# Optimization experiments

Hardware: AMD Instinct MI355X
Metric: run time of the kernel (lower is better)

Reference implementation:

```python
import jax, jax.numpy as jnp
import numpy as np

N = 50000
E = 800000
IN_DIM = 256
HID = 32
HEADS = 4
OUT_DIM = 40
NEG_SLOPE = 0.2


def gat_layer(x, src, dst, W, a_src, a_dst, b, n_nodes, heads, ch, concat):
    # x: [N, F_in], W: [F_in, heads*ch], a_src/a_dst: [heads, ch], b: [out]
    h = (x @ W).reshape(n_nodes, heads, ch)                 # [N,H,C]
    alpha_s = jnp.einsum('nhc,hc->nh', h, a_src)            # [N,H]
    alpha_d = jnp.einsum('nhc,hc->nh', h, a_dst)            # [N,H]
    e = jax.nn.leaky_relu(alpha_s[src] + alpha_d[dst], NEG_SLOPE)  # [E,H]
    # segment softmax over destination neighborhoods (self-loops guarantee nonempty)
    m = jax.ops.segment_max(e, dst, num_segments=n_nodes)   # [N,H]
    e = jnp.exp(e - m[dst])
    denom = jax.ops.segment_sum(e, dst, num_segments=n_nodes)
    alpha = e / (denom[dst] + 1e-16)                         # [E,H]
    msg = h[src] * alpha[:, :, None]                         # [E,H,C]
    out = jax.ops.segment_sum(msg, dst, num_segments=n_nodes)  # [N,H,C]
    out = out.reshape(n_nodes, heads * ch) if concat else out.mean(axis=1)
    return out + b


def setup_inputs() -> dict:
    key = jax.random.key(0)
    ks = jax.random.split(key, 10)
    x = jax.random.normal(ks[0], (N, IN_DIM), dtype=jnp.float32)
    edge_index = jax.random.randint(ks[1], (2, E), 0, N, dtype=jnp.int32)
    s1 = 1.0 / np.sqrt(IN_DIM)
    s2 = 1.0 / np.sqrt(HID * HEADS)
    return {
        'x': x,
        'edge_index': edge_index,
        'W1': jax.random.normal(ks[2], (IN_DIM, HEADS * HID), dtype=jnp.float32) * s1,
        'a_src1': jax.random.normal(ks[3], (HEADS, HID), dtype=jnp.float32) * s1,
        'a_dst1': jax.random.normal(ks[4], (HEADS, HID), dtype=jnp.float32) * s1,
        'b1': jnp.zeros((HEADS * HID,), dtype=jnp.float32),
        'W2': jax.random.normal(ks[5], (HEADS * HID, OUT_DIM), dtype=jnp.float32) * s2,
        'a_src2': jax.random.normal(ks[6], (1, OUT_DIM), dtype=jnp.float32) * s2,
        'a_dst2': jax.random.normal(ks[7], (1, OUT_DIM), dtype=jnp.float32) * s2,
        'b2': jnp.zeros((OUT_DIM,), dtype=jnp.float32),
    }


def reference(x, edge_index, W1, a_src1, a_dst1, b1, W2, a_src2, a_dst2, b2):
    # PyG GATConv adds self-loops by default
    loops = jnp.arange(N, dtype=edge_index.dtype)
    src = jnp.concatenate([edge_index[0], loops])
    dst = jnp.concatenate([edge_index[1], loops])
    h = gat_layer(x, src, dst, W1, a_src1, a_dst1, b1, N, HEADS, HID, True)
    h = jax.nn.relu(h)
    out = gat_layer(h, src, dst, W2, a_src2, a_dst2, b2, N, 1, OUT_DIM, False)
    return jax.nn.log_softmax(out, axis=1)
```

## Files before the change

### kernel.cpp

```cpp
#include <hip/hip_runtime.h>
#include <math.h>

#define N_NODES 50000
#define N_EDGES 800000
#define IN_DIM  256
#define F1      128
#define HEADS   4
#define OUT_DIM 40
#define NEG     0.2f

#define NB   391
#define CAP  3072
#define EB   4096

#define DCAP 96

typedef __attribute__((ext_vector_type(8))) short short8;
typedef __attribute__((ext_vector_type(4))) float float4v;

__device__ __forceinline__ unsigned short f2bf(float f) {
  unsigned int u = __float_as_uint(f);
  u += 0x7FFF + ((u >> 16) & 1);
  return (unsigned short)(u >> 16);
}
__device__ __forceinline__ float bf2f(unsigned short h) {
  return __uint_as_float((unsigned int)h << 16);
}
__device__ __forceinline__ float bflo(unsigned int u) { return __uint_as_float(u << 16); }
__device__ __forceinline__ float bfhi(unsigned int u) { return __uint_as_float(u & 0xffff0000u); }

__device__ __forceinline__ float lrelu(float e) { return e > 0.f ? e : e * NEG; }

__device__ __forceinline__ void gload_lds16(const void* g, void* l) {
  __builtin_amdgcn_global_load_lds(
      (const __attribute__((address_space(1))) unsigned int*)g,
      (__attribute__((address_space(3))) unsigned int*)l, 16, 0, 0);
}

__global__ __launch_bounds__(256) void bin_kernel(const int* __restrict__ ei,
                                                  int* __restrict__ gcnt,
                                                  int2* __restrict__ gbucket) {
  __shared__ int ls[EB];
  __shared__ int ld[EB];
  __shared__ int lcnt[NB];
  __shared__ int lcur[NB];
  __shared__ int gbaseS[NB];
  int tid = threadIdx.x;
  size_t base = (size_t)blockIdx.x * EB;
  for (int t = tid; t < NB; t += 256) { lcnt[t] = 0; lcur[t] = 0; }
  __syncthreads();
#pragma unroll
  for (int l = 0; l < EB / 256; l++) {
    int li = l * 256 + tid;
    size_t idx = base + li;
    int s = 0, d = -1;
    if (idx < N_EDGES) {
      s = ei[idx];
      d = ei[N_EDGES + idx];
      atomicAdd(&lcnt[d >> 7], 1);
    }
    ls[li] = s;
    ld[li] = d;
  }
  __syncthreads();
  for (int t = tid; t < NB; t += 256) gbaseS[t] = atomicAdd(&gcnt[t], lcnt[t]);
  __syncthreads();
#pragma unroll
  for (int l = 0; l < EB / 256; l++) {
    int li = l * 256 + tid;
    int d = ld[li];
    if (d >= 0) {
      int b = d >> 7;
      int r = gbaseS[b] + atomicAdd(&lcur[b], 1);
      if (r >= CAP) r = CAP - 1;
      gbucket[(size_t)b * CAP + r] = make_int2(ls[li], d);
    }
  }
}

__global__ __launch_bounds__(512) void bucketscan_kernel(const int* __restrict__ gcnt,
                                                         int* __restrict__ bbase,
                                                         int* __restrict__ row_ptr) {
  __shared__ int lds[512];
  int tid = threadIdx.x;
  int v = (tid < NB) ? gcnt[tid] : 0;
  lds[tid] = v;
  __syncthreads();
  for (int off = 1; off < 512; off <<= 1) {
    int t = (tid >= off) ? lds[tid - off] : 0;
    __syncthreads();
    lds[tid] += t;
    __syncthreads();
  }
  if (tid < NB) bbase[tid] = lds[tid] - v;
  if (tid == 0) row_ptr[N_NODES] = N_EDGES;
}

__global__ __launch_bounds__(256) void csr_kernel(const int2* __restrict__ gbucket,
                                                  const int* __restrict__ gcnt,
                                                  const int* __restrict__ bbase,
                                                  int* __restrict__ row_ptr,
                                                  int* __restrict__ col) {
  __shared__ int2 ent[CAP];
  __shared__ int hcnt[128];
  __shared__ int sc[128];
  __shared__ int cur[128];
  int b = blockIdx.x;
  int tid = threadIdx.x;
  int cnt = gcnt[b]; if (cnt > CAP) cnt = CAP;
  int base = bbase[b];
  if (tid < 128) hcnt[tid] = 0;
  __syncthreads();
  for (int i = tid; i < cnt; i += 256) {
    int2 e = gbucket[(size_t)b * CAP + i];
    ent[i] = e;
    atomicAdd(&hcnt[e.y & 127], 1);
  }
  __syncthreads();
  if (tid < 128) sc[tid] = hcnt[tid];
  __syncthreads();
  for (int off = 1; off < 128; off <<= 1) {
    int t = 0;
    if (tid < 128 && tid >= off) t = sc[tid - off];
    __syncthreads();
    if (tid < 128) sc[tid] += t;
    __syncthreads();
  }
  if (tid < 128) {
    int excl = sc[tid] - hcnt[tid];
    cur[tid] = excl;
    int node = (b << 7) + tid;
    if (node < N_NODES) row_ptr[node] = base + excl;
  }
  __syncthreads();
  for (int i = tid; i < cnt; i += 256) {
    int2 e = ent[i];
    int r = atomicAdd(&cur[e.y & 127], 1);
    col[base + r] = e.x;
  }
}

__global__ __launch_bounds__(256) void w1pack_kernel(const float* __restrict__ W1,
                                                     unsigned short* __restrict__ wHi,
                                                     unsigned short* __restrict__ wLo) {
  int tid = blockIdx.x * 256 + threadIdx.x;
  int kk = tid >> 9;
  int rest = tid & 511;
  int t = rest >> 6;
  int lane = rest & 63;
  int q = lane >> 4;
  int ln = lane & 15;
  int n = t * 16 + ln;
  unsigned int hi[4], lo[4];
#pragma unroll
  for (int jj = 0; jj < 4; jj++) {
    unsigned short h0, h1, l0, l1;
    {
      float v = W1[(kk * 32 + q * 8 + jj * 2) * F1 + n];
      h0 = f2bf(v); l0 = f2bf(v - bf2f(h0));
    }
    {
      float v = W1[(kk * 32 + q * 8 + jj * 2 + 1) * F1 + n];
      h1 = f2bf(v); l1 = f2bf(v - bf2f(h1));
    }
    hi[jj] = (unsigned int)h0 | ((unsigned int)h1 << 16);
    lo[jj] = (unsigned int)l0 | ((unsigned int)l1 << 16);
  }
  size_t base = (size_t)tid * 8;
  *(uint4*)&wHi[base] = make_uint4(hi[0], hi[1], hi[2], hi[3]);
  *(uint4*)&wLo[base] = make_uint4(lo[0], lo[1], lo[2], lo[3]);
}

__global__ __launch_bounds__(256) void gemm1_mfma_kernel(
    const float* __restrict__ x, const unsigned short* __restrict__ wHi,
    const unsigned short* __restrict__ wLo,
    const float* __restrict__ a_src, const float* __restrict__ a_dst,
    unsigned short* __restrict__ h1b, float* __restrict__ as1, float* __restrict__ ad1) {
  __shared__ short8 Bsh[2][1024];
  int tid = threadIdx.x;
  int w = tid >> 6;
  int lane = tid & 63;
  int q = lane >> 4;
  int ln = lane & 15;
  int rowBase = blockIdx.x * 64 + w * 16;
  int rowA = rowBase + ln;
  int rowAc = rowA < N_NODES ? rowA : N_NODES - 1;
  float4v acc[8];
#pragma unroll
  for (int t = 0; t < 8; t++) acc[t] = (float4v){0.f, 0.f, 0.f, 0.f};
  const short8* bhp = (const short8*)wHi;
  const short8* blp = (const short8*)wLo;

  auto prefetch = [&](int kk, int buf) {
#pragma unroll
    for (int c = 0; c < 2; c++) {
      int chunk = w * 2 + c;
      gload_lds16(bhp + (size_t)kk * 512 + chunk * 64 + lane, &Bsh[buf][chunk * 64]);
      gload_lds16(blp + (size_t)kk * 512 + chunk * 64 + lane, &Bsh[buf][512 + chunk * 64]);
    }
  };

  const float4* xbase = (const float4*)(x + (size_t)rowAc * IN_DIM + q * 8);
  float4 a0 = xbase[0];
  float4 a1 = xbase[1];
  prefetch(0, 0);
  __syncthreads();

#pragma unroll 1
  for (int kk = 0; kk < 8; kk++) {
    int buf = kk & 1;
    if (kk < 7) prefetch(kk + 1, buf ^ 1);
    int kn = (kk < 7) ? kk + 1 : 7;
    float4 n0 = xbase[kn * 8];
    float4 n1 = xbase[kn * 8 + 1];
    float av[8] = {a0.x, a0.y, a0.z, a0.w, a1.x, a1.y, a1.z, a1.w};
    short8 ahi, alo;
#pragma unroll
    for (int j = 0; j < 8; j++) {
      unsigned short hh = f2bf(av[j]);
      ahi[j] = (short)hh;
      alo[j] = (short)f2bf(av[j] - bf2f(hh));
    }
    const short8* bs = &Bsh[buf][0];
#pragma unroll
    for (int t = 0; t < 8; t++) {
      short8 bh = bs[t * 64 + lane];
      short8 bl = bs[512 + t * 64 + lane];
      acc[t] = __builtin_amdgcn_mfma_f32_16x16x32_bf16(ahi, bh, acc[t], 0, 0, 0);
      acc[t] = __builtin_amdgcn_mfma_f32_16x16x32_bf16(ahi, bl, acc[t], 0, 0, 0);
      acc[t] = __builtin_amdgcn_mfma_f32_16x16x32_bf16(alo, bh, acc[t], 0, 0, 0);
    }
    a0 = n0;
    a1 = n1;
    if (kk < 7) __syncthreads();
  }

  float asv[8], adv[8];
#pragma unroll
  for (int t = 0; t < 8; t++) {
    asv[t] = a_src[t * 16 + ln];
    adv[t] = a_dst[t * 16 + ln];
  }
#pragma unroll
  for (int reg = 0; reg < 4; reg++) {
    int r = rowBase + q * 4 + reg;
    bool valid = (r < N_NODES);
    if (valid) {
#pragma unroll
      for (int t = 0; t < 8; t++)
        h1b[(size_t)r * F1 + t * 16 + ln] = f2bf(acc[t][reg]);
    }
#pragma unroll
    for (int h = 0; h < 4; h++) {
      float sa = acc[2 * h][reg] * asv[2 * h] + acc[2 * h + 1][reg] * asv[2 * h + 1];
      float sd = acc[2 * h][reg] * adv[2 * h] + acc[2 * h + 1][reg] * adv[2 * h + 1];
#pragma unroll
      for (int off = 1; off < 16; off <<= 1) {
        sa += __shfl_xor(sa, off);
        sd += __shfl_xor(sd, off);
      }
      if (ln == 0 && valid) {
        as1[r * 4 + h] = sa;
        ad1[r * 4 + h] = sd;
      }
    }
  }
}

__global__ __launch_bounds__(256) void gather1_kernel(
    const unsigned short* __restrict__ h1b, const float* __restrict__ as1,
    const float* __restrict__ ad1, const float* __restrict__ b1,
    const int* __restrict__ row_ptr, const int* __restrict__ col,
    float* __restrict__ x2) {
  __shared__ float4 wsh[4][DCAP];
  __shared__ int ssh[4][DCAP];
  int wv = threadIdx.x >> 6;
  int n = blockIdx.x * 4 + wv;
  if (n >= N_NODES) return;
  int lane = threadIdx.x & 63;
  int start = row_ptr[n];
  int deg = row_ptr[n + 1] - start;
  bool fast = (deg + 1) <= DCAP;
  float4 ad = *(const float4*)&ad1[n * 4];
  float s0 = 0.f, s1 = 0.f, s2 = 0.f, s3 = 0.f;
  for (int i = lane; i <= deg; i += 64) {
    int src = (i < deg) ? col[start + i] : n;
    float4 as = *(const float4*)&as1[src * 4];
    float e0 = __expf(lrelu(as.x + ad.x));
    float e1 = __expf(lrelu(as.y + ad.y));
    float e2 = __expf(lrelu(as.z + ad.z));
    float e3 = __expf(lrelu(as.w + ad.w));
    s0 += e0; s1 += e1; s2 += e2; s3 += e3;
    if (fast) {
      ssh[wv][i] = src;
      wsh[wv][i] = make_float4(e0, e1, e2, e3);
    }
  }
#pragma unroll
  for (int off = 32; off > 0; off >>= 1) {
    s0 += __shfl_xor(s0, off);
    s1 += __shfl_xor(s1, off);
    s2 += __shfl_xor(s2, off);
    s3 += __shfl_xor(s3, off);
  }
  int slot = lane >> 4;
  int lane16 = lane & 15;
  int head = lane16 >> 2;
  float rsh = (head == 0) ? s0 : (head == 1) ? s1 : (head == 2) ? s2 : s3;
  rsh = 1.f / (rsh + 1e-16f);
  float4 accA = make_float4(0.f, 0.f, 0.f, 0.f);
  float4 accB = make_float4(0.f, 0.f, 0.f, 0.f);
  if (fast) {
    const float* wp = (const float*)&wsh[wv][0];
    int i = slot;
    for (; i + 4 <= deg; i += 8) {
      int sA = ssh[wv][i];
      int sB = ssh[wv][i + 4];
      float wA = wp[i * 4 + head] * rsh;
      float wB = wp[(i + 4) * 4 + head] * rsh;
      uint4 uA = *(const uint4*)(h1b + (size_t)sA * F1 + lane16 * 8);
      uint4 uB = *(const uint4*)(h1b + (size_t)sB * F1 + lane16 * 8);
      accA.x += wA * bflo(uA.x); accA.y += wA * bfhi(uA.x);
      accA.z += wA * bflo(uA.y); accA.w += wA * bfhi(uA.y);
      accB.x += wA * bflo(uA.z); accB.y += wA * bfhi(uA.z);
      accB.z += wA * bflo(uA.w); accB.w += wA * bfhi(uA.w);
      accA.x += wB * bflo(uB.x); accA.y += wB * bfhi(uB.x);
      accA.z += wB * bflo(uB.y); accA.w += wB * bfhi(uB.y);
      accB.x += wB * bflo(uB.z); accB.y += wB * bfhi(uB.z);
      accB.z += wB * bflo(uB.w); accB.w += wB * bfhi(uB.w);
    }
    if (i <= deg) {
      int s = ssh[wv][i];
      float w = wp[i * 4 + head] * rsh;
      uint4 u = *(const uint4*)(h1b + (size_t)s * F1 + lane16 * 8);
      accA.x += w * bflo(u.x); accA.y += w * bfhi(u.x);
      accA.z += w * bflo(u.y); accA.w += w * bfhi(u.y);
      accB.x += w * bflo(u.z); accB.y += w * bfhi(u.z);
      accB.z += w * bflo(u.w); accB.w += w * bfhi(u.w);
    }
  } else {
    float adh = (head == 0) ? ad.x : (head == 1) ? ad.y : (head == 2) ? ad.z : ad.w;
    for (int i = slot; i <= deg; i += 4) {
      int src = (i < deg) ? col[start + i] : n;
      float w = __expf(lrelu(as1[src * 4 + head] + adh)) * rsh;
      uint4 u = *(const uint4*)(h1b + (size_t)src * F1 + lane16 * 8);
      accA.x += w * bflo(u.x); accA.y += w * bfhi(u.x);
      accA.z += w * bflo(u.y); accA.w += w * bfhi(u.y);
      accB.x += w * bflo(u.z); accB.y += w * bfhi(u.z);
      accB.z += w * bflo(u.w); accB.w += w * bfhi(u.w);
    }
  }
#pragma unroll
  for (int off = 16; off <= 32; off <<= 1) {
    accA.x += __shfl_xor(accA.x, off); accA.y += __shfl_xor(accA.y, off);
    accA.z += __shfl_xor(accA.z, off); accA.w += __shfl_xor(accA.w, off);
    accB.x += __shfl_xor(accB.x, off); accB.y += __shfl_xor(accB.y, off);
    accB.z += __shfl_xor(accB.z, off); accB.w += __shfl_xor(accB.w, off);
  }
  if (slot == 0) {
    float4 bA = *(const float4*)&b1[lane16 * 8];
    float4 bB = *(const float4*)&b1[lane16 * 8 + 4];
    float4 oA, oB;
    oA.x = fmaxf(accA.x + bA.x, 0.f); oA.y = fmaxf(accA.y + bA.y, 0.f);
    oA.z = fmaxf(accA.z + bA.z, 0.f); oA.w = fmaxf(accA.w + bA.w, 0.f);
    oB.x = fmaxf(accB.x + bB.x, 0.f); oB.y = fmaxf(accB.y + bB.y, 0.f);
    oB.z = fmaxf(accB.z + bB.z, 0.f); oB.w = fmaxf(accB.w + bB.w, 0.f);
    *(float4*)&x2[(size_t)n * F1 + lane16 * 8] = oA;
    *(float4*)&x2[(size_t)n * F1 + lane16 * 8 + 4] = oB;
  }
}

__global__ __launch_bounds__(256) void gemm2_kernel(
    const float* __restrict__ x2, const float* __restrict__ W2,
    const float* __restrict__ asv, const float* __restrict__ adv,
    unsigned short* __restrict__ h2b, float* __restrict__ as2, float* __restrict__ ad2) {
  __shared__ float xs[64][132];
  __shared__ float W2s[128][44];
  __shared__ float asv_s[40], adv_s[40];
  int tid = threadIdx.x;
  int bm = blockIdx.x * 64;
#pragma unroll
  for (int l = 0; l < 8; l++) {
    int idx = tid + l * 256;
    int r = idx >> 5;
    int c4 = (idx & 31) << 2;
    float4 v = make_float4(0.f, 0.f, 0.f, 0.f);
    if (bm + r < N_NODES) v = *(const float4*)&x2[(size_t)(bm + r) * F1 + c4];
    *(float4*)&xs[r][c4] = v;
  }
#pragma unroll
  for (int l = 0; l < 5; l++) {
    int idx = tid + l * 256;
    int k = idx / 10;
    int c4 = (idx - k * 10) * 4;
    *(float4*)&W2s[k][c4] = *(const float4*)&W2[k * OUT_DIM + c4];
  }
  if (tid < OUT_DIM) { asv_s[tid] = asv[tid]; adv_s[tid] = adv[tid]; }
  __syncthreads();
  int r = tid >> 2;
  int cb = (tid & 3) * 10;
  float acc[10] = {0.f};
  for (int k = 0; k < F1; k++) {
    float xv = xs[r][k];
#pragma unroll
    for (int c = 0; c < 10; c++) acc[c] += xv * W2s[k][cb + c];
  }
  int grow = bm + r;
  float sa = 0.f, sd = 0.f;
#pragma unroll
  for (int c = 0; c < 10; c++) {
    sa += acc[c] * asv_s[cb + c];
    sd += acc[c] * adv_s[cb + c];
  }
#pragma unroll
  for (int off = 1; off < 4; off <<= 1) {
    sa += __shfl_xor(sa, off);
    sd += __shfl_xor(sd, off);
  }
  if (grow < N_NODES) {
#pragma unroll
    for (int c = 0; c < 10; c += 2) {
      unsigned int p = ((unsigned int)f2bf(acc[c + 1]) << 16) | f2bf(acc[c]);
      *(unsigned int*)&h2b[(size_t)grow * OUT_DIM + cb + c] = p;
    }
    if ((tid & 3) == 0) { as2[grow] = sa; ad2[grow] = sd; }
  }
}

__global__ __launch_bounds__(256) void gather2_kernel(
    const unsigned short* __restrict__ h2b, const float* __restrict__ as2,
    const float* __restrict__ ad2, const float* __restrict__ b2,
    const int* __restrict__ row_ptr, const int* __restrict__ col,
    float* __restrict__ out) {
  __shared__ float w2sh[4][DCAP];
  __shared__ int s2sh[4][DCAP];
  int wv = threadIdx.x >> 6;
  int n = blockIdx.x * 4 + wv;
  if (n >= N_NODES) return;
  int lane = threadIdx.x & 63;
  int start = row_ptr[n];
  int deg = row_ptr[n + 1] - start;
  bool fast = (deg + 1) <= DCAP;
  float adh = ad2[n];
  float part = 0.f;
  for (int i = lane; i <= deg; i += 64) {
    int src = (i < deg) ? col[start + i] : n;
    float e = __expf(lrelu(as2[src] + adh));
    part += e;
    if (fast) { s2sh[wv][i] = src; w2sh[wv][i] = e; }
  }
#pragma unroll
  for (int off = 32; off > 0; off >>= 1) part += __shfl_xor(part, off);
  float rs = 1.f / (part + 1e-16f);
  int slot = lane / 5;
  int c = lane - slot * 5;
  float4 accA = make_float4(0.f, 0.f, 0.f, 0.f);
  float4 accB = make_float4(0.f, 0.f, 0.f, 0.f);
  if (slot < 12) {
    if (fast) {
      for (int i = slot; i <= deg; i += 12) {
        int src = s2sh[wv][i];
        float wgt = w2sh[wv][i] * rs;
        uint4 u = *(const uint4*)(h2b + (size_t)src * OUT_DIM + c * 8);
        accA.x += wgt * bflo(u.x); accA.y += wgt * bfhi(u.x);
        accA.z += wgt * bflo(u.y); accA.w += wgt * bfhi(u.y);
        accB.x += wgt * bflo(u.z); accB.y += wgt * bfhi(u.z);
        accB.z += wgt * bflo(u.w); accB.w += wgt * bfhi(u.w);
      }
    } else {
      for (int i = slot; i <= deg; i += 12) {
        int src = (i < deg) ? col[start + i] : n;
        float wgt = __expf(lrelu(as2[src] + adh)) * rs;
        uint4 u = *(const uint4*)(h2b + (size_t)src * OUT_DIM + c * 8);
        accA.x += wgt * bflo(u.x); accA.y += wgt * bfhi(u.x);
        accA.z += wgt * bflo(u.y); accA.w += wgt * bfhi(u.y);
        accB.x += wgt * bflo(u.z); accB.y += wgt * bfhi(u.z);
        accB.z += wgt * bflo(u.w); accB.w += wgt * bfhi(u.w);
      }
    }
  }
  {
    float v[8] = {accA.x, accA.y, accA.z, accA.w, accB.x, accB.y, accB.z, accB.w};
#pragma unroll
    for (int k = 0; k < 8; k++) v[k] += __shfl(v[k], lane + 30);
#pragma unroll
    for (int k = 0; k < 8; k++) v[k] += __shfl(v[k], lane + 15);
    float t1[8], t2[8];
#pragma unroll
    for (int k = 0; k < 8; k++) t1[k] = __shfl(v[k], lane + 5);
#pragma unroll
    for (int k = 0; k < 8; k++) t2[k] = __shfl(v[k], lane + 10);
#pragma unroll
    for (int k = 0; k < 8; k++) v[k] += t1[k] + t2[k];
    accA.x = v[0]; accA.y = v[1]; accA.z = v[2]; accA.w = v[3];
    accB.x = v[4]; accB.y = v[5]; accB.z = v[6]; accB.w = v[7];
  }
  bool owner = (slot == 0);
  float vals[8] = {accA.x, accA.y, accA.z, accA.w, accB.x, accB.y, accB.z, accB.w};
  float lmax = -1e30f, lsum = 0.f;
  if (owner) {
#pragma unroll
    for (int k = 0; k < 8; k++) {
      vals[k] += b2[c * 8 + k];
      lmax = fmaxf(lmax, vals[k]);
    }
  }
  float gmax = lmax;
#pragma unroll
  for (int off = 32; off > 0; off >>= 1) gmax = fmaxf(gmax, __shfl_xor(gmax, off));
  if (owner) {
#pragma unroll
    for (int k = 0; k < 8; k++) lsum += __expf(vals[k] - gmax);
  }
#pragma unroll
  for (int off = 32; off > 0; off >>= 1) lsum += __shfl_xor(lsum, off);
  if (owner) {
    float lse = gmax + __logf(lsum);
    float4 oA = make_float4(vals[0] - lse, vals[1] - lse, vals[2] - lse, vals[3] - lse);
    float4 oB = make_float4(vals[4] - lse, vals[5] - lse, vals[6] - lse, vals[7] - lse);
    *(float4*)&out[(size_t)n * OUT_DIM + c * 8] = oA;
    *(float4*)&out[(size_t)n * OUT_DIM + c * 8 + 4] = oB;
  }
}

extern "C" void kernel_launch(void* const* d_in, const int* in_sizes, int n_in,
                              void* d_out, int out_size, void* d_ws, size_t ws_size,
                              hipStream_t stream) {
  const float* x      = (const float*)d_in[0];
  const int*   ei     = (const int*)d_in[1];
  const float* W1     = (const float*)d_in[2];
  const float* a_src1 = (const float*)d_in[3];
  const float* a_dst1 = (const float*)d_in[4];
  const float* b1     = (const float*)d_in[5];
  const float* W2     = (const float*)d_in[6];
  const float* a_src2 = (const float*)d_in[7];
  const float* a_dst2 = (const float*)d_in[8];
  const float* b2     = (const float*)d_in[9];
  float* out = (float*)d_out;

  char* ws = (char*)d_ws;
  size_t off = 0;
  auto alloc = [&](size_t bytes) -> void* {
    void* p = ws + off;
    off += (bytes + 255) & ~(size_t)255;
    return p;
  };
  unsigned short* h1b = (unsigned short*)alloc((size_t)N_NODES * F1 * 2);
  unsigned short* h2b = (unsigned short*)alloc((size_t)N_NODES * OUT_DIM * 2);
  unsigned short* wHi = (unsigned short*)alloc((size_t)IN_DIM * F1 * 2);
  unsigned short* wLo = (unsigned short*)alloc((size_t)IN_DIM * F1 * 2);
  float* as1    = (float*)alloc((size_t)N_NODES * HEADS * 4);
  float* ad1    = (float*)alloc((size_t)N_NODES * HEADS * 4);
  float* x2     = (float*)alloc((size_t)N_NODES * F1 * 4);
  float* as2    = (float*)alloc((size_t)N_NODES * 4);
  float* ad2    = (float*)alloc((size_t)N_NODES * 4);
  int* row_ptr  = (int*)alloc((size_t)(N_NODES + 1) * 4);
  int* col      = (int*)alloc((size_t)N_EDGES * 4);
  int* gcnt     = (int*)alloc((size_t)NB * 4);
  int* bbase    = (int*)alloc((size_t)NB * 4);
  int2* gbucket = (int2*)alloc((size_t)NB * CAP * 8);

  hipMemsetAsync(gcnt, 0, (size_t)NB * 4, stream);
  bin_kernel<<<(N_EDGES + EB - 1) / EB, 256, 0, stream>>>(ei, gcnt, gbucket);
  bucketscan_kernel<<<1, 512, 0, stream>>>(gcnt, bbase, row_ptr);
  csr_kernel<<<NB, 256, 0, stream>>>(gbucket, gcnt, bbase, row_ptr, col);

  w1pack_kernel<<<16, 256, 0, stream>>>(W1, wHi, wLo);
  gemm1_mfma_kernel<<<(N_NODES + 63) / 64, 256, 0, stream>>>(
      x, wHi, wLo, a_src1, a_dst1, h1b, as1, ad1);
  gather1_kernel<<<(N_NODES + 3) / 4, 256, 0, stream>>>(h1b, as1, ad1, b1, row_ptr, col, x2);

  gemm2_kernel<<<(N_NODES + 63) / 64, 256, 0, stream>>>(x2, W2, a_src2, a_dst2, h2b, as2, ad2);
  gather2_kernel<<<(N_NODES + 3) / 4, 256, 0, stream>>>(h2b, as2, ad2, b2, row_ptr, col, out);
}
```

Before: 251.0 us.

## Merge preprocessing kernels and run CSR build alongside GEMM1 in one launch

Five launches become two. W1 packing and edge binning are merged into one grid split by block index. GEMM1 and CSR construction are merged into another, and each CSR block computes its own bucket base with a block reduction over gcnt, so the separate scan kernel is removed. This cuts launch gaps and lets the independent graph-build work overlap the GEMM. The cost is that every CSR block redundantly re-sums the bucket prefix, and LDS is sized for the larger of the two roles.

```diff
diff --git a/kernel.cpp b/kernel.cpp
--- a/kernel.cpp
+++ b/kernel.cpp
@@ -12,6 +12,8 @@
 #define NB   391
 #define CAP  3072
 #define EB   4096
+#define PREW 16
+#define G1B  782
 
 #define DCAP 96
 
@@ -37,232 +39,223 @@
       (__attribute__((address_space(3))) unsigned int*)l, 16, 0, 0);
 }
 
-__global__ __launch_bounds__(256) void bin_kernel(const int* __restrict__ ei,
+__global__ __launch_bounds__(256) void pre_kernel(const float* __restrict__ W1,
+                                                  unsigned short* __restrict__ wHi,
+                                                  unsigned short* __restrict__ wLo,
+                                                  const int* __restrict__ ei,
                                                   int* __restrict__ gcnt,
                                                   int2* __restrict__ gbucket) {
-  __shared__ int ls[EB];
-  __shared__ int ld[EB];
-  __shared__ int lcnt[NB];
-  __shared__ int lcur[NB];
-  __shared__ int gbaseS[NB];
-  int tid = threadIdx.x;
-  size_t base = (size_t)blockIdx.x * EB;
-  for (int t = tid; t < NB; t += 256) { lcnt[t] = 0; lcur[t] = 0; }
-  __syncthreads();
-#pragma unroll
-  for (int l = 0; l < EB / 256; l++) {
-    int li = l * 256 + tid;
-    size_t idx = base + li;
-    int s = 0, d = -1;
-    if (idx < N_EDGES) {
-      s = ei[idx];
-      d = ei[N_EDGES + idx];
-      atomicAdd(&lcnt[d >> 7], 1);
-    }
-    ls[li] = s;
-    ld[li] = d;
-  }
-  __syncthreads();
-  for (int t = tid; t < NB; t += 256) gbaseS[t] = atomicAdd(&gcnt[t], lcnt[t]);
-  __syncthreads();
-#pragma unroll
-  for (int l = 0; l < EB / 256; l++) {
-    int li = l * 256 + tid;
-    int d = ld[li];
-    if (d >= 0) {
-      int b = d >> 7;
-      int r = gbaseS[b] + atomicAdd(&lcur[b], 1);
-      if (r >= CAP) r = CAP - 1;
-      gbucket[(size_t)b * CAP + r] = make_int2(ls[li], d);
-    }
-  }
-}
-
-__global__ __launch_bounds__(512) void bucketscan_kernel(const int* __restrict__ gcnt,
-                                                         int* __restrict__ bbase,
-                                                         int* __restrict__ row_ptr) {
-  __shared__ int lds[512];
-  int tid = threadIdx.x;
-  int v = (tid < NB) ? gcnt[tid] : 0;
-  lds[tid] = v;
-  __syncthreads();
-  for (int off = 1; off < 512; off <<= 1) {
-    int t = (tid >= off) ? lds[tid - off] : 0;
-    __syncthreads();
-    lds[tid] += t;
-    __syncthreads();
-  }
-  if (tid < NB) bbase[tid] = lds[tid] - v;
-  if (tid == 0) row_ptr[N_NODES] = N_EDGES;
-}
-
-__global__ __launch_bounds__(256) void csr_kernel(const int2* __restrict__ gbucket,
-                                                  const int* __restrict__ gcnt,
-                                                  const int* __restrict__ bbase,
-                                                  int* __restrict__ row_ptr,
-                                                  int* __restrict__ col) {
-  __shared__ int2 ent[CAP];
-  __shared__ int hcnt[128];
-  __shared__ int sc[128];
-  __shared__ int cur[128];
-  int b = blockIdx.x;
-  int tid = threadIdx.x;
-  int cnt = gcnt[b]; if (cnt > CAP) cnt = CAP;
-  int base = bbase[b];
-  if (tid < 128) hcnt[tid] = 0;
-  __syncthreads();
-  for (int i = tid; i < cnt; i += 256) {
-    int2 e = gbucket[(size_t)b * CAP + i];
-    ent[i] = e;
-    atomicAdd(&hcnt[e.y & 127], 1);
-  }
-  __syncthreads();
-  if (tid < 128) sc[tid] = hcnt[tid];
-  __syncthreads();
-  for (int off = 1; off < 128; off <<= 1) {
-    int t = 0;
-    if (tid < 128 && tid >= off) t = sc[tid - off];
-    __syncthreads();
-    if (tid < 128) sc[tid] += t;
-    __syncthreads();
-  }
-  if (tid < 128) {
-    int excl = sc[tid] - hcnt[tid];
-    cur[tid] = excl;
-    int node = (b << 7) + tid;
-    if (node < N_NODES) row_ptr[node] = base + excl;
-  }
-  __syncthreads();
-  for (int i = tid; i < cnt; i += 256) {
-    int2 e = ent[i];
-    int r = atomicAdd(&cur[e.y & 127], 1);
-    col[base + r] = e.x;
-  }
-}
-
-__global__ __launch_bounds__(256) void w1pack_kernel(const float* __restrict__ W1,
-                                                     unsigned short* __restrict__ wHi,
-                                                     unsigned short* __restrict__ wLo) {
-  int tid = blockIdx.x * 256 + threadIdx.x;
-  int kk = tid >> 9;
-  int rest = tid & 511;
-  int t = rest >> 6;
-  int lane = rest & 63;
-  int q = lane >> 4;
-  int ln = lane & 15;
-  int n = t * 16 + ln;
-  unsigned int hi[4], lo[4];
-#pragma unroll
-  for (int jj = 0; jj < 4; jj++) {
-    unsigned short h0, h1, l0, l1;
-    {
-      float v = W1[(kk * 32 + q * 8 + jj * 2) * F1 + n];
-      h0 = f2bf(v); l0 = f2bf(v - bf2f(h0));
-    }
-    {
-      float v = W1[(kk * 32 + q * 8 + jj * 2 + 1) * F1 + n];
-      h1 = f2bf(v); l1 = f2bf(v - bf2f(h1));
-    }
-    hi[jj] = (unsigned int)h0 | ((unsigned int)h1 << 16);
-    lo[jj] = (unsigned int)l0 | ((unsigned int)l1 << 16);
-  }
-  size_t base = (size_t)tid * 8;
-  *(uint4*)&wHi[base] = make_uint4(hi[0], hi[1], hi[2], hi[3]);
-  *(uint4*)&wLo[base] = make_uint4(lo[0], lo[1], lo[2], lo[3]);
-}
-
-__global__ __launch_bounds__(256) void gemm1_mfma_kernel(
+  __shared__ int smem[EB * 2 + NB * 3];
+  if (blockIdx.x < PREW) {
+    int tid = blockIdx.x * 256 + threadIdx.x;
+    int kk = tid >> 9;
+    int rest = tid & 511;
+    int t = rest >> 6;
+    int lane = rest & 63;
+    int q = lane >> 4;
+    int ln = lane & 15;
+    int n = t * 16 + ln;
+    unsigned int hi[4], lo[4];
+#pragma unroll
+    for (int jj = 0; jj < 4; jj++) {
+      unsigned short h0, h1, l0, l1;
+      {
+        float v = W1[(kk * 32 + q * 8 + jj * 2) * F1 + n];
+        h0 = f2bf(v); l0 = f2bf(v - bf2f(h0));
+      }
+      {
+        float v = W1[(kk * 32 + q * 8 + jj * 2 + 1) * F1 + n];
+        h1 = f2bf(v); l1 = f2bf(v - bf2f(h1));
+      }
+      hi[jj] = (unsigned int)h0 | ((unsigned int)h1 << 16);
+      lo[jj] = (unsigned int)l0 | ((unsigned int)l1 << 16);
+    }
+    size_t base = (size_t)tid * 8;
+    *(uint4*)&wHi[base] = make_uint4(hi[0], hi[1], hi[2], hi[3]);
+    *(uint4*)&wLo[base] = make_uint4(lo[0], lo[1], lo[2], lo[3]);
+  } else {
+    int* ls = smem;
+    int* ld = smem + EB;
+    int* lcnt = smem + 2 * EB;
+    int* lcur = lcnt + NB;
+    int* gbaseS = lcur + NB;
+    int tid = threadIdx.x;
+    size_t base = (size_t)(blockIdx.x - PREW) * EB;
+    for (int t = tid; t < NB; t += 256) { lcnt[t] = 0; lcur[t] = 0; }
+    __syncthreads();
+#pragma unroll
+    for (int l = 0; l < EB / 256; l++) {
+      int li = l * 256 + tid;
+      size_t idx = base + li;
+      int s = 0, d = -1;
+      if (idx < N_EDGES) {
+        s = ei[idx];
+        d = ei[N_EDGES + idx];
+        atomicAdd(&lcnt[d >> 7], 1);
+      }
+      ls[li] = s;
+      ld[li] = d;
+    }
+    __syncthreads();
+    for (int t = tid; t < NB; t += 256) gbaseS[t] = atomicAdd(&gcnt[t], lcnt[t]);
+    __syncthreads();
+#pragma unroll
+    for (int l = 0; l < EB / 256; l++) {
+      int li = l * 256 + tid;
+      int d = ld[li];
+      if (d >= 0) {
+        int b = d >> 7;
+        int r = gbaseS[b] + atomicAdd(&lcur[b], 1);
+        if (r >= CAP) r = CAP - 1;
+        gbucket[(size_t)b * CAP + r] = make_int2(ls[li], d);
+      }
+    }
+  }
+}
+
+__global__ __launch_bounds__(256) void mid_kernel(
     const float* __restrict__ x, const unsigned short* __restrict__ wHi,
     const unsigned short* __restrict__ wLo,
     const float* __restrict__ a_src, const float* __restrict__ a_dst,
-    unsigned short* __restrict__ h1b, float* __restrict__ as1, float* __restrict__ ad1) {
-  __shared__ short8 Bsh[2][1024];
-  int tid = threadIdx.x;
-  int w = tid >> 6;
-  int lane = tid & 63;
-  int q = lane >> 4;
-  int ln = lane & 15;
-  int rowBase = blockIdx.x * 64 + w * 16;
-  int rowA = rowBase + ln;
-  int rowAc = rowA < N_NODES ? rowA : N_NODES - 1;
-  float4v acc[8];
-#pragma unroll
-  for (int t = 0; t < 8; t++) acc[t] = (float4v){0.f, 0.f, 0.f, 0.f};
-  const short8* bhp = (const short8*)wHi;
-  const short8* blp = (const short8*)wLo;
-
-  auto prefetch = [&](int kk, int buf) {
-#pragma unroll
-    for (int c = 0; c < 2; c++) {
-      int chunk = w * 2 + c;
-      gload_lds16(bhp + (size_t)kk * 512 + chunk * 64 + lane, &Bsh[buf][chunk * 64]);
-      gload_lds16(blp + (size_t)kk * 512 + chunk * 64 + lane, &Bsh[buf][512 + chunk * 64]);
-    }
-  };
-
-  const float4* xbase = (const float4*)(x + (size_t)rowAc * IN_DIM + q * 8);
-  float4 a0 = xbase[0];
-  float4 a1 = xbase[1];
-  prefetch(0, 0);
-  __syncthreads();
+    unsigned short* __restrict__ h1b, float* __restrict__ as1, float* __restrict__ ad1,
+    const int2* __restrict__ gbucket, const int* __restrict__ gcnt,
+    int* __restrict__ row_ptr, int* __restrict__ col) {
+  __shared__ short8 smem[2048];
+  if (blockIdx.x < G1B) {
+    short8 (*Bsh)[1024] = (short8(*)[1024])smem;
+    int bid = blockIdx.x;
+    int tid = threadIdx.x;
+    int w = tid >> 6;
+    int lane = tid & 63;
+    int q = lane >> 4;
+    int ln = lane & 15;
+    int rowBase = bid * 64 + w * 16;
+    int rowA = rowBase + ln;
+    int rowAc = rowA < N_NODES ? rowA : N_NODES - 1;
+    float4v acc[8];
+#pragma unroll
+    for (int t = 0; t < 8; t++) acc[t] = (float4v){0.f, 0.f, 0.f, 0.f};
+    const short8* bhp = (const short8*)wHi;
+    const short8* blp = (const short8*)wLo;
+
+    auto prefetch = [&](int kk, int buf) {
+#pragma unroll
+      for (int c = 0; c < 2; c++) {
+        int chunk = w * 2 + c;
+        gload_lds16(bhp + (size_t)kk * 512 + chunk * 64 + lane, &Bsh[buf][chunk * 64]);
+        gload_lds16(blp + (size_t)kk * 512 + chunk * 64 + lane, &Bsh[buf][512 + chunk * 64]);
+      }
+    };
+
+    const float4* xbase = (const float4*)(x + (size_t)rowAc * IN_DIM + q * 8);
+    float4 a0 = xbase[0];
+    float4 a1 = xbase[1];
+    prefetch(0, 0);
+    __syncthreads();
 
 #pragma unroll 1
-  for (int kk = 0; kk < 8; kk++) {
-    int buf = kk & 1;
-    if (kk < 7) prefetch(kk + 1, buf ^ 1);
-    int kn = (kk < 7) ? kk + 1 : 7;
-    float4 n0 = xbase[kn * 8];
-    float4 n1 = xbase[kn * 8 + 1];
-    float av[8] = {a0.x, a0.y, a0.z, a0.w, a1.x, a1.y, a1.z, a1.w};
-    short8 ahi, alo;
-#pragma unroll
-    for (int j = 0; j < 8; j++) {
-      unsigned short hh = f2bf(av[j]);
-      ahi[j] = (short)hh;
-      alo[j] = (short)f2bf(av[j] - bf2f(hh));
-    }
-    const short8* bs = &Bsh[buf][0];
+    for (int kk = 0; kk < 8; kk++) {
+      int buf = kk & 1;
+      if (kk < 7) prefetch(kk + 1, buf ^ 1);
+      int kn = (kk < 7) ? kk + 1 : 7;
+      float4 n0 = xbase[kn * 8];
+      float4 n1 = xbase[kn * 8 + 1];
+      float av[8] = {a0.x, a0.y, a0.z, a0.w, a1.x, a1.y, a1.z, a1.w};
+      short8 ahi, alo;
+#pragma unroll
+      for (int j = 0; j < 8; j++) {
+        unsigned short hh = f2bf(av[j]);
+        ahi[j] = (short)hh;
+        alo[j] = (short)f2bf(av[j] - bf2f(hh));
+      }
+      const short8* bs = &Bsh[buf][0];
+#pragma unroll
+      for (int t = 0; t < 8; t++) {
+        short8 bh = bs[t * 64 + lane];
+        short8 bl = bs[512 + t * 64 + lane];
+        acc[t] = __builtin_amdgcn_mfma_f32_16x16x32_bf16(ahi, bh, acc[t], 0, 0, 0);
+        acc[t] = __builtin_amdgcn_mfma_f32_16x16x32_bf16(ahi, bl, acc[t], 0, 0, 0);
+        acc[t] = __builtin_amdgcn_mfma_f32_16x16x32_bf16(alo, bh, acc[t], 0, 0, 0);
+      }
+      a0 = n0;
+      a1 = n1;
+      if (kk < 7) __syncthreads();
+    }
+
+    float asv[8], adv[8];
 #pragma unroll
     for (int t = 0; t < 8; t++) {
-      short8 bh = bs[t * 64 + lane];
-      short8 bl = bs[512 + t * 64 + lane];
-      acc[t] = __builtin_amdgcn_mfma_f32_16x16x32_bf16(ahi, bh, acc[t], 0, 0, 0);
-      acc[t] = __builtin_amdgcn_mfma_f32_16x16x32_bf16(ahi, bl, acc[t], 0, 0, 0);
-      acc[t] = __builtin_amdgcn_mfma_f32_16x16x32_bf16(alo, bh, acc[t], 0, 0, 0);
-    }
-    a0 = n0;
-    a1 = n1;
-    if (kk < 7) __syncthreads();
-  }
-
-  float asv[8], adv[8];
-#pragma unroll
-  for (int t = 0; t < 8; t++) {
-    asv[t] = a_src[t * 16 + ln];
-    adv[t] = a_dst[t * 16 + ln];
-  }
-#pragma unroll
-  for (int reg = 0; reg < 4; reg++) {
-    int r = rowBase + q * 4 + reg;
-    bool valid = (r < N_NODES);
-    if (valid) {
-#pragma unroll
-      for (int t = 0; t < 8; t++)
-        h1b[(size_t)r * F1 + t * 16 + ln] = f2bf(acc[t][reg]);
-    }
-#pragma unroll
-    for (int h = 0; h < 4; h++) {
-      float sa = acc[2 * h][reg] * asv[2 * h] + acc[2 * h + 1][reg] * asv[2 * h + 1];
-      float sd = acc[2 * h][reg] * adv[2 * h] + acc[2 * h + 1][reg] * adv[2 * h + 1];
-#pragma unroll
-      for (int off = 1; off < 16; off <<= 1) {
-        sa += __shfl_xor(sa, off);
-        sd += __shfl_xor(sd, off);
-      }
-      if (ln == 0 && valid) {
-        as1[r * 4 + h] = sa;
-        ad1[r * 4 + h] = sd;
-      }
+      asv[t] = a_src[t * 16 + ln];
+      adv[t] = a_dst[t * 16 + ln];
+    }
+#pragma unroll
+    for (int reg = 0; reg < 4; reg++) {
+      int r = rowBase + q * 4 + reg;
+      bool valid = (r < N_NODES);
+      if (valid) {
+#pragma unroll
+        for (int t = 0; t < 8; t++)
+          h1b[(size_t)r * F1 + t * 16 + ln] = f2bf(acc[t][reg]);
+      }
+#pragma unroll
+      for (int h = 0; h < 4; h++) {
+        float sa = acc[2 * h][reg] * asv[2 * h] + acc[2 * h + 1][reg] * asv[2 * h + 1];
+        float sd = acc[2 * h][reg] * adv[2 * h] + acc[2 * h + 1][reg] * adv[2 * h + 1];
+#pragma unroll
+        for (int off = 1; off < 16; off <<= 1) {
+          sa += __shfl_xor(sa, off);
+          sd += __shfl_xor(sd, off);
+        }
+        if (ln == 0 && valid) {
+          as1[r * 4 + h] = sa;
+          ad1[r * 4 + h] = sd;
+        }
+      }
+    }
+  } else {
+    int2* ent = (int2*)smem;
+    int* hcnt = (int*)(ent + CAP);
+    int* sc   = hcnt + 128;
+    int* cur  = sc + 128;
+    int* red  = cur + 128;
+    int b = blockIdx.x - G1B;
+    int tid = threadIdx.x;
+    int cnt = gcnt[b]; if (cnt > CAP) cnt = CAP;
+    if (tid < 128) hcnt[tid] = 0;
+    int part = 0;
+    for (int i = tid; i < b; i += 256) part += gcnt[i];
+#pragma unroll
+    for (int off = 32; off > 0; off >>= 1) part += __shfl_xor(part, off);
+    if ((tid & 63) == 0) red[tid >> 6] = part;
+    __syncthreads();
+    int base = red[0] + red[1] + red[2] + red[3];
+    for (int i = tid; i < cnt; i += 256) {
+      int2 e = gbucket[(size_t)b * CAP + i];
+      ent[i] = e;
+      atomicAdd(&hcnt[e.y & 127], 1);
+    }
+    __syncthreads();
+    if (tid < 128) sc[tid] = hcnt[tid];
+    __syncthreads();
+    for (int off = 1; off < 128; off <<= 1) {
+      int t = 0;
+      if (tid < 128 && tid >= off) t = sc[tid - off];
+      __syncthreads();
+      if (tid < 128) sc[tid] += t;
+      __syncthreads();
+    }
+    if (tid < 128) {
+      int excl = sc[tid] - hcnt[tid];
+      cur[tid] = excl;
+      int node = (b << 7) + tid;
+      if (node < N_NODES) row_ptr[node] = base + excl;
+    }
+    if (b == 0 && tid == 0) row_ptr[N_NODES] = N_EDGES;
+    __syncthreads();
+    for (int i = tid; i < cnt; i += 256) {
+      int2 e = ent[i];
+      int r = atomicAdd(&cur[e.y & 127], 1);
+      col[base + r] = e.x;
     }
   }
 }
@@ -557,17 +550,12 @@
   int* row_ptr  = (int*)alloc((size_t)(N_NODES + 1) * 4);
   int* col      = (int*)alloc((size_t)N_EDGES * 4);
   int* gcnt     = (int*)alloc((size_t)NB * 4);
-  int* bbase    = (int*)alloc((size_t)NB * 4);
   int2* gbucket = (int2*)alloc((size_t)NB * CAP * 8);
 
   hipMemsetAsync(gcnt, 0, (size_t)NB * 4, stream);
-  bin_kernel<<<(N_EDGES + EB - 1) / EB, 256, 0, stream>>>(ei, gcnt, gbucket);
-  bucketscan_kernel<<<1, 512, 0, stream>>>(gcnt, bbase, row_ptr);
-  csr_kernel<<<NB, 256, 0, stream>>>(gbucket, gcnt, bbase, row_ptr, col);
-
-  w1pack_kernel<<<16, 256, 0, stream>>>(W1, wHi, wLo);
-  gemm1_mfma_kernel<<<(N_NODES + 63) / 64, 256, 0, stream>>>(
-      x, wHi, wLo, a_src1, a_dst1, h1b, as1, ad1);
+  pre_kernel<<<PREW + (N_EDGES + EB - 1) / EB, 256, 0, stream>>>(W1, wHi, wLo, ei, gcnt, gbucket);
+  mid_kernel<<<G1B + NB, 256, 0, stream>>>(x, wHi, wLo, a_src1, a_dst1, h1b, as1, ad1,
+                                           gbucket, gcnt, row_ptr, col);
   gather1_kernel<<<(N_NODES + 3) / 4, 256, 0, stream>>>(h1b, as1, ad1, b1, row_ptr, col, x2);
 
   gemm2_kernel<<<(N_NODES + 63) / 64, 256, 0, stream>>>(x2, W2, a_src2, a_dst2, h2b, as2, ad2);
```

After: 241.8 us. -3.6%, faster.
